# Performance work log

Measured on AMD Instinct MI355X. Metric: run time of the kernel, lower is better.

The kernel has to match this reference:

```python
import jax, jax.numpy as jnp
import numpy as np

# module constants (from init_kwargs)
OUT_W = 22
OUT_H = 48
IN_H = 64
IN_W = 44
DT_OFF = 0.5
DX_OFF = 0.5
DY_OFF = 0.5
SIGMA_OFF = 1.0
DELTA_T_OFF = 1.0
DELTA_OFF = 1.0
EPS = 1e-8
ATT_H = int(round(OUT_W / IN_W * IN_H))  # 32

N, C, T, H, W = 16, 64, 30, 64, 44


def setup_inputs() -> dict:
    key = jax.random.key(0)
    ks = jax.random.split(key, 8)
    inp = {"x": jax.random.normal(ks[0], (N, C, T, H, W), dtype=jnp.float32)}
    names = ["dt", "dx", "dy", "log_sigma2", "log_delta_t", "log_delta", "log_gamma"]
    for i, nm in enumerate(names):
        inp[nm] = jax.random.normal(ks[i + 1], (N, 1), dtype=jnp.float32)
    return inp


def _filterbank(mu, grid_len, sigma2):
    # mu: [N, out_len]; sigma2: [N,1,1] -> F: [N, out_len, grid_len], row-normalized
    g = jnp.arange(grid_len, dtype=jnp.float32)  # [grid_len]
    F = jnp.exp(-((g[None, None, :] - mu[:, :, None]) ** 2) / (2.0 * sigma2))
    return F / jnp.maximum(F.sum(axis=2, keepdims=True), EPS)


def reference(x, dt, dx, dy, log_sigma2, log_delta_t, log_delta, log_gamma):
    n, c, t, h, w = x.shape
    anchor_t, anchor_x, anchor_y = t * DT_OFF, w * DX_OFF, h * DY_OFF

    dt_ = jnp.tanh(dt) * t / 2.0 + anchor_t          # [N,1]
    dx_ = jnp.tanh(dx) * IN_W / 2.0 + anchor_x
    dy_ = jnp.tanh(dy) * IN_H / 2.0 + anchor_y
    sigma2 = (jnp.exp(log_sigma2) * SIGMA_OFF).reshape(-1, 1, 1)
    delta_t = jnp.exp(log_delta_t) * DELTA_T_OFF
    delta = jnp.exp(log_delta) * DELTA_OFF
    gamma = jax.nn.sigmoid(log_gamma)

    gt = jnp.arange(t, dtype=jnp.float32)[None, :]
    gx = jnp.arange(OUT_W, dtype=jnp.float32)[None, :]
    gy = jnp.arange(ATT_H, dtype=jnp.float32)[None, :]
    mu_t = dt_ + (gt - t / 2.0) * delta_t            # [N,T]
    mu_x = dx_ + (gx - OUT_W / 2.0) * delta          # [N,out_w]
    mu_y = dy_ + (gy - ATT_H / 2.0) * delta          # [N,att_h]

    Ft = _filterbank(mu_t, t, sigma2)                # [N,T,T]
    Fx = _filterbank(mu_x, w, sigma2)                # [N,out_w,W]
    Fy = _filterbank(mu_y, h, sigma2)                # [N,att_h,H]

    # glimpse = Ft @ (Fy @ x @ Fx^T) over appropriate axes
    g = jnp.einsum('ncthw,naw->nctha', x, Fx)        # [N,C,T,H,out_w]
    g = jnp.einsum('nctha,nbh->nctba', g, Fy)        # [N,C,T,att_h,out_w]
    g = jnp.einsum('nctba,nst->ncsba', g, Ft)        # [N,C,T,att_h,out_w]

    out = g * gamma.reshape(-1, 1, 1, 1, 1)
    pad_t = (OUT_H - ATT_H) // 2
    pad_b = OUT_H - pad_t - ATT_H
    out = jnp.pad(out, ((0, 0), (0, 0), (0, 0), (pad_t, pad_b), (0, 0)))
    return out
```

## Files before the change

### kernel.cpp

```cpp
#include <hip/hip_runtime.h>
#include <hip/hip_fp16.h>

#define XN 16
#define XC 64
#define XT 30
#define XH 64
#define XW 44
#define OUTW 22
#define ATTH 32
#define OUTH 48
#define SLICE (XH*XW)
#define OSLICE (OUTH*OUTW)

#define WS_FX 0
#define WS_FY (3*64*4)
#define WS_FT (WS_FY + 4*64*4)
#define WS_N  (WS_FT + 2*64*4)

typedef _Float16 f16;
typedef f16 f16x8 __attribute__((ext_vector_type(8)));
typedef float f32x16 __attribute__((ext_vector_type(16)));
typedef float f32x4 __attribute__((ext_vector_type(4)));

__device__ __forceinline__ unsigned int PK(float a, float b) {
    return __builtin_bit_cast(unsigned int, __builtin_amdgcn_cvt_pkrtz(a, b));
}
__device__ __forceinline__ f32x16 MF(uint4 a, uint4 b, f32x16 c) {
    return __builtin_amdgcn_mfma_f32_32x32x16_f16(
        __builtin_bit_cast(f16x8, a), __builtin_bit_cast(f16x8, b), c, 0, 0, 0);
}
__device__ __forceinline__ f32x16 ZF() {
    f32x16 z;
    #pragma unroll
    for (int i = 0; i < 16; ++i) z[i] = 0.f;
    return z;
}

__global__ void prep_kernel(const float* __restrict__ dtp, const float* __restrict__ dxp,
                            const float* __restrict__ dyp, const float* __restrict__ ls2,
                            const float* __restrict__ ldt, const float* __restrict__ ldp,
                            unsigned int* __restrict__ ws)
{
    __shared__ float fx[22][44];
    __shared__ float fy[32][64];
    __shared__ float ft[30][32];
    const int n = blockIdx.x;
    const int r = threadIdx.x;
    const float dt_ = tanhf(dtp[n]) * 15.f + 15.f;
    const float dx_ = tanhf(dxp[n]) * 22.f + 22.f;
    const float dy_ = tanhf(dyp[n]) * 32.f + 32.f;
    const float inv2s = 1.f / (2.f * expf(ls2[n]));
    const float delta_t = expf(ldt[n]);
    const float delta = expf(ldp[n]);

    if (r < 30) {
        float mu = dt_ + (float)(r - 15) * delta_t;
        float e[30]; float sum = 0.f;
        for (int t = 0; t < 30; ++t) { float d = (float)t - mu; float v = expf(-d*d*inv2s); e[t] = v; sum += v; }
        float inv = 1.f / fmaxf(sum, 1e-8f);
        for (int t = 0; t < 30; ++t) ft[r][t] = e[t] * inv;
        ft[r][30] = 0.f; ft[r][31] = 0.f;
    } else if (r < 52) {
        int a = r - 30;
        float mu = dx_ + (float)(a - 11) * delta;
        float e[44]; float sum = 0.f;
        for (int w = 0; w < 44; ++w) { float d = (float)w - mu; float v = expf(-d*d*inv2s); e[w] = v; sum += v; }
        float inv = 1.f / fmaxf(sum, 1e-8f);
        for (int w = 0; w < 44; ++w) fx[a][w] = e[w] * inv;
    } else if (r < 84) {
        int b = r - 52;
        float mu = dy_ + (float)(b - 16) * delta;
        float e[64]; float sum = 0.f;
        for (int h = 0; h < 64; ++h) { float d = (float)h - mu; float v = expf(-d*d*inv2s); e[h] = v; sum += v; }
        float inv = 1.f / fmaxf(sum, 1e-8f);
        for (int h = 0; h < 64; ++h) fy[b][h] = e[h] * inv;
    }
    __syncthreads();

    if (r < 64) {
        const int al = r & 31, hf = r >> 5;
        unsigned int* wn = ws + n * WS_N;
        #pragma unroll
        for (int kt = 0; kt < 3; ++kt) {
            int w0 = kt*16 + 8*hf;
            float v[8];
            #pragma unroll
            for (int i = 0; i < 8; ++i) { int w = w0 + i; v[i] = (al < 22 && w < 44) ? fx[al][w] : 0.f; }
            #pragma unroll
            for (int j = 0; j < 4; ++j) {
                unsigned int lo = __half_as_ushort(__float2half_rn(v[2*j]));
                unsigned int hi = __half_as_ushort(__float2half_rn(v[2*j+1]));
                wn[WS_FX + (kt*64 + r)*4 + j] = lo | (hi << 16);
            }
        }
        #pragma unroll
        for (int kt = 0; kt < 4; ++kt) {
            int h0 = kt*16 + 8*hf;
            float v[8];
            #pragma unroll
            for (int i = 0; i < 8; ++i) v[i] = fy[al][h0 + i];
            #pragma unroll
            for (int j = 0; j < 4; ++j) {
                unsigned int lo = __half_as_ushort(__float2half_rn(v[2*j]));
                unsigned int hi = __half_as_ushort(__float2half_rn(v[2*j+1]));
                wn[WS_FY + (kt*64 + r)*4 + j] = lo | (hi << 16);
            }
        }
        #pragma unroll
        for (int kt = 0; kt < 2; ++kt) {
            int t0 = kt*16 + 8*hf;
            float v[8];
            #pragma unroll
            for (int i = 0; i < 8; ++i) v[i] = (al < 30) ? ft[al][t0 + i] : 0.f;
            #pragma unroll
            for (int j = 0; j < 4; ++j) {
                unsigned int lo = __half_as_ushort(__float2half_rn(v[2*j]));
                unsigned int hi = __half_as_ushort(__float2half_rn(v[2*j+1]));
                wn[WS_FT + (kt*64 + r)*4 + j] = lo | (hi << 16);
            }
        }
    }
}

__global__ __launch_bounds__(256, 3) void glimpse_kernel(
    const float* __restrict__ x, const unsigned int* __restrict__ ws,
    const float* __restrict__ p_lg, float* __restrict__ out)
{
    const int tid = threadIdx.x;
    const int n = blockIdx.x >> 6, c = blockIdx.x & 63;
    const int wv = tid >> 6, l = tid & 63;
    const int al = l & 31, hf = l >> 5;

    __shared__ unsigned int a2t[704*17];

    for (int r = tid; r < 704; r += 256) { a2t[r*17 + 15] = 0u; a2t[r*17 + 16] = 0u; }

    const size_t obase = (size_t)(n*XC + c) * (XT*OSLICE);
    {
        f32x4 z4 = {0.f, 0.f, 0.f, 0.f};
        f32x4* out4 = (f32x4*)(out + obase);
        #pragma unroll
        for (int k2 = 0; k2 < 11; ++k2) {
            int idx = tid + k2*256;
            if (idx < 2640) {
                int s = idx / 88;
                int rr = idx - s*88;
                int j = (rr < 44) ? rr : (rr + 176);
                __builtin_nontemporal_store(z4, out4 + s*264 + j);
            }
        }
    }

    const unsigned int* wn = ws + n * WS_N;
    uint4 fxf[3], fyf[4], ftf[2];
    #pragma unroll
    for (int kt = 0; kt < 3; ++kt) fxf[kt] = *(const uint4*)(wn + WS_FX + (kt*64 + l)*4);
    #pragma unroll
    for (int kt = 0; kt < 4; ++kt) fyf[kt] = *(const uint4*)(wn + WS_FY + (kt*64 + l)*4);
    #pragma unroll
    for (int kt = 0; kt < 2; ++kt) ftf[kt] = *(const uint4*)(wn + WS_FT + (kt*64 + l)*4);

    const float gamma = 1.f / (1.f + expf(-p_lg[n]));

    unsigned short* a2t16 = (unsigned short*)a2t;
    const float* xc = x + (size_t)(n*XC + c) * (XT*SLICE);

    #pragma unroll 1
    for (int t = wv; t < XT; t += 4) {
        const float* xs = xc + (size_t)t * SLICE;
        const float* rb0 = xs + al*44;
        const float* rb1 = xs + (32 + al)*44;
        float4 A0a = *(const float4*)(rb0 + 8*hf);
        float4 A1a = *(const float4*)(rb0 + 8*hf + 4);
        float4 B0a = *(const float4*)(rb0 + 16 + 8*hf);
        float4 B1a = *(const float4*)(rb0 + 16 + 8*hf + 4);
        float4 C0a = *(const float4*)(rb0 + 32 + 8*hf);
        float4 C1a = (hf == 0) ? *(const float4*)(rb0 + 36) : make_float4(0.f,0.f,0.f,0.f);
        float4 A0b = *(const float4*)(rb1 + 8*hf);
        float4 A1b = *(const float4*)(rb1 + 8*hf + 4);
        float4 B0b = *(const float4*)(rb1 + 16 + 8*hf);
        float4 B1b = *(const float4*)(rb1 + 16 + 8*hf + 4);
        float4 C0b = *(const float4*)(rb1 + 32 + 8*hf);
        float4 C1b = (hf == 0) ? *(const float4*)(rb1 + 36) : make_float4(0.f,0.f,0.f,0.f);

        f32x16 D0 = ZF(), D1m = ZF(), D2 = ZF();
        {
            uint4 u0 = make_uint4(PK(A0a.x,A0a.y), PK(A0a.z,A0a.w), PK(A1a.x,A1a.y), PK(A1a.z,A1a.w));
            uint4 u1 = make_uint4(PK(B0a.x,B0a.y), PK(B0a.z,B0a.w), PK(B1a.x,B1a.y), PK(B1a.z,B1a.w));
            uint4 u2 = make_uint4(PK(C0a.x,C0a.y), PK(C0a.z,C0a.w), PK(C1a.x,C1a.y), PK(C1a.z,C1a.w));
            D0 = MF(u0, fxf[0], D0); D0 = MF(u1, fxf[1], D0); D0 = MF(u2, fxf[2], D0);
        }
        {
            uint4 u0 = make_uint4(PK(A0b.x,A0b.y), PK(A0b.z,A0b.w), PK(A1b.x,A1b.y), PK(A1b.z,A1b.w));
            uint4 u1 = make_uint4(PK(B0b.x,B0b.y), PK(B0b.z,B0b.w), PK(B1b.x,B1b.y), PK(B1b.z,B1b.w));
            uint4 u2 = make_uint4(PK(C0b.x,C0b.y), PK(C0b.z,C0b.w), PK(C1b.x,C1b.y), PK(C1b.z,C1b.w));
            D1m = MF(u0, fxf[0], D1m); D1m = MF(u1, fxf[1], D1m); D1m = MF(u2, fxf[2], D1m);
        }

        #pragma unroll
        for (int half = 0; half < 2; ++half) {
            const f32x16& D = half ? D1m : D0;
            unsigned int w0g[4], w1g[4];
            #pragma unroll
            for (int g = 0; g < 4; ++g) {
                w0g[g] = PK(D[4*g],   D[4*g+1]);
                w1g[g] = PK(D[4*g+2], D[4*g+3]);
            }
            #pragma unroll
            for (int ktl = 0; ktl < 2; ++ktl) {
                const int gA = 2*ktl, gB = 2*ktl + 1;
                unsigned int own0 = hf ? w0g[gB] : w0g[gA];
                unsigned int own1 = hf ? w1g[gB] : w1g[gA];
                unsigned int snd0 = hf ? w0g[gA] : w0g[gB];
                unsigned int snd1 = hf ? w1g[gA] : w1g[gB];
                unsigned int rcv0 = (unsigned int)__shfl_xor((int)snd0, 32, 64);
                unsigned int rcv1 = (unsigned int)__shfl_xor((int)snd1, 32, 64);
                uint4 frag;
                frag.x = hf ? rcv0 : own0;
                frag.y = hf ? rcv1 : own1;
                frag.z = hf ? own0 : rcv0;
                frag.w = hf ? own1 : rcv1;
                D2 = MF(fyf[half*2 + ktl], frag, D2);
            }
        }

        if (al < 22) {
            #pragma unroll
            for (int q = 0; q < 16; ++q) {
                int b = (q & 3) + 8*(q >> 2) + 4*hf;
                unsigned short hv = __builtin_bit_cast(unsigned short, (_Float16)D2[q]);
                a2t16[(b*22 + al)*34 + t] = hv;
            }
        }
    }
    __syncthreads();

    #pragma unroll 2
    for (int nt = wv; nt < 22; nt += 4) {
        int ba = nt*32 + al;
        f32x16 D3 = ZF();
        #pragma unroll
        for (int kt = 0; kt < 2; ++kt) {
            int base = ba*17 + kt*8 + 4*hf;
            uint4 bw;
            bw.x = a2t[base]; bw.y = a2t[base+1]; bw.z = a2t[base+2]; bw.w = a2t[base+3];
            D3 = MF(ftf[kt], bw, D3);
        }
        float* ob = out + obase + 176 + ba;
        #pragma unroll
        for (int q = 0; q < 16; ++q) {
            int s = (q & 3) + 8*(q >> 2) + 4*hf;
            if (s < XT) __builtin_nontemporal_store(gamma * D3[q], ob + s*OSLICE);
        }
    }
}

extern "C" void kernel_launch(void* const* d_in, const int* in_sizes, int n_in,
                              void* d_out, int out_size, void* d_ws, size_t ws_size,
                              hipStream_t stream) {
    const float* x   = (const float*)d_in[0];
    const float* dt  = (const float*)d_in[1];
    const float* dx  = (const float*)d_in[2];
    const float* dy  = (const float*)d_in[3];
    const float* ls2 = (const float*)d_in[4];
    const float* ldt = (const float*)d_in[5];
    const float* ld  = (const float*)d_in[6];
    const float* lg  = (const float*)d_in[7];
    float* out = (float*)d_out;
    unsigned int* ws = (unsigned int*)d_ws;

    prep_kernel<<<dim3(XN), dim3(96), 0, stream>>>(dt, dx, dy, ls2, ldt, ld, ws);
    glimpse_kernel<<<dim3(XN * XC), dim3(256), 0, stream>>>(x, ws, lg, out);
}
```

Baseline: 116.5 us.

## Coalesce x loads, prefetch next slice, stage through swizzled per-wave LDS

Each wave now loads its T-slice of x as fully coalesced float4 chunks (11 per lane), packs them to fp16 and writes them into a per-wave swizzled LDS tile. The MFMA A-operands are then read back from LDS instead of coming from strided row-wise global loads. The next slice's loads are issued before the current slice is processed, as a register double-buffer. This is meant to remove uncoalesced global access and hide load latency, at the cost of extra LDS traffic and more registers, which is why the occupancy hint drops from 3 to 2 blocks.

```diff
diff --git a/kernel.cpp b/kernel.cpp
--- a/kernel.cpp
+++ b/kernel.cpp
@@ -122,7 +122,7 @@
     }
 }
 
-__global__ __launch_bounds__(256, 3) void glimpse_kernel(
+__global__ __launch_bounds__(256, 2) void glimpse_kernel(
     const float* __restrict__ x, const unsigned int* __restrict__ ws,
     const float* __restrict__ p_lg, float* __restrict__ out)
 {
@@ -131,9 +131,15 @@
     const int wv = tid >> 6, l = tid & 63;
     const int al = l & 31, hf = l >> 5;
 
-    __shared__ unsigned int a2t[704*17];
+    __shared__ unsigned int lds_all[4*1024 + 704*17];
+    unsigned int* xst = lds_all + wv * 1024;
+    unsigned int* a2t = lds_all + 4096;
 
     for (int r = tid; r < 704; r += 256) { a2t[r*17 + 15] = 0u; a2t[r*17 + 16] = 0u; }
+    if (l < 32) {
+        int ph = l*32 + ((5 ^ (l & 7)) << 2) + 2;
+        xst[ph] = 0u; xst[ph + 1] = 0u;
+    }
 
     const size_t obase = (size_t)(n*XC + c) * (XT*OSLICE);
     {
@@ -165,35 +171,60 @@
     unsigned short* a2t16 = (unsigned short*)a2t;
     const float* xc = x + (size_t)(n*XC + c) * (XT*SLICE);
 
+    float4 v[11];
+    {
+        const float4* src = (const float4*)(xc + (size_t)wv * SLICE);
+        #pragma unroll
+        for (int k = 0; k < 11; ++k) v[k] = src[k*64 + l];
+    }
+
     #pragma unroll 1
     for (int t = wv; t < XT; t += 4) {
-        const float* xs = xc + (size_t)t * SLICE;
-        const float* rb0 = xs + al*44;
-        const float* rb1 = xs + (32 + al)*44;
-        float4 A0a = *(const float4*)(rb0 + 8*hf);
-        float4 A1a = *(const float4*)(rb0 + 8*hf + 4);
-        float4 B0a = *(const float4*)(rb0 + 16 + 8*hf);
-        float4 B1a = *(const float4*)(rb0 + 16 + 8*hf + 4);
-        float4 C0a = *(const float4*)(rb0 + 32 + 8*hf);
-        float4 C1a = (hf == 0) ? *(const float4*)(rb0 + 36) : make_float4(0.f,0.f,0.f,0.f);
-        float4 A0b = *(const float4*)(rb1 + 8*hf);
-        float4 A1b = *(const float4*)(rb1 + 8*hf + 4);
-        float4 B0b = *(const float4*)(rb1 + 16 + 8*hf);
-        float4 B1b = *(const float4*)(rb1 + 16 + 8*hf + 4);
-        float4 C0b = *(const float4*)(rb1 + 32 + 8*hf);
-        float4 C1b = (hf == 0) ? *(const float4*)(rb1 + 36) : make_float4(0.f,0.f,0.f,0.f);
+        unsigned int pk[22];
+        #pragma unroll
+        for (int k = 0; k < 11; ++k) {
+            pk[2*k]   = PK(v[k].x, v[k].y);
+            pk[2*k+1] = PK(v[k].z, v[k].w);
+        }
+        if (t + 4 < XT) {
+            const float4* src = (const float4*)(xc + (size_t)(t+4) * SLICE);
+            #pragma unroll
+            for (int k = 0; k < 11; ++k) v[k] = src[k*64 + l];
+        }
 
         f32x16 D0 = ZF(), D1m = ZF(), D2 = ZF();
+        #pragma unroll
+        for (int k = 0; k < 6; ++k) {
+            int flat = k*64 + l;
+            if (k < 5 || l < 32) {
+                int r = flat / 11;
+                int m = flat - r*11;
+                int ph = (r & 31)*32 + (((m >> 1) ^ (r & 7)) << 2) + ((m & 1) << 1);
+                uint2 pr; pr.x = pk[2*k]; pr.y = pk[2*k+1];
+                *(uint2*)(xst + ph) = pr;
+            }
+        }
         {
-            uint4 u0 = make_uint4(PK(A0a.x,A0a.y), PK(A0a.z,A0a.w), PK(A1a.x,A1a.y), PK(A1a.z,A1a.w));
-            uint4 u1 = make_uint4(PK(B0a.x,B0a.y), PK(B0a.z,B0a.w), PK(B1a.x,B1a.y), PK(B1a.z,B1a.w));
-            uint4 u2 = make_uint4(PK(C0a.x,C0a.y), PK(C0a.z,C0a.w), PK(C1a.x,C1a.y), PK(C1a.z,C1a.w));
+            uint4 u0 = *(const uint4*)(xst + al*32 + (((0 + hf) ^ (al & 7)) << 2));
+            uint4 u1 = *(const uint4*)(xst + al*32 + (((2 + hf) ^ (al & 7)) << 2));
+            uint4 u2 = *(const uint4*)(xst + al*32 + (((4 + hf) ^ (al & 7)) << 2));
             D0 = MF(u0, fxf[0], D0); D0 = MF(u1, fxf[1], D0); D0 = MF(u2, fxf[2], D0);
         }
+        #pragma unroll
+        for (int k = 5; k < 11; ++k) {
+            int flat = k*64 + l;
+            if (k > 5 || l >= 32) {
+                int r = flat / 11;
+                int m = flat - r*11;
+                int ph = (r & 31)*32 + (((m >> 1) ^ (r & 7)) << 2) + ((m & 1) << 1);
+                uint2 pr; pr.x = pk[2*k]; pr.y = pk[2*k+1];
+                *(uint2*)(xst + ph) = pr;
+            }
+        }
         {
-            uint4 u0 = make_uint4(PK(A0b.x,A0b.y), PK(A0b.z,A0b.w), PK(A1b.x,A1b.y), PK(A1b.z,A1b.w));
-            uint4 u1 = make_uint4(PK(B0b.x,B0b.y), PK(B0b.z,B0b.w), PK(B1b.x,B1b.y), PK(B1b.z,B1b.w));
-            uint4 u2 = make_uint4(PK(C0b.x,C0b.y), PK(C0b.z,C0b.w), PK(C1b.x,C1b.y), PK(C1b.z,C1b.w));
+            uint4 u0 = *(const uint4*)(xst + al*32 + (((0 + hf) ^ (al & 7)) << 2));
+            uint4 u1 = *(const uint4*)(xst + al*32 + (((2 + hf) ^ (al & 7)) << 2));
+            uint4 u2 = *(const uint4*)(xst + al*32 + (((4 + hf) ^ (al & 7)) << 2));
             D1m = MF(u0, fxf[0], D1m); D1m = MF(u1, fxf[1], D1m); D1m = MF(u2, fxf[2], D1m);
         }
 
```

New measurement: 113.1 us. -2.9%, faster.

## Use 512-thread blocks and batch two time-slice loads per wave

Applied to the files above, without the earlier changes.

Doubles the block to 8 waves, so each (n,c) block spreads its 30 time slices over more waves. Each wave now issues the global loads for two time slices (t and t+8) up front before running the MFMA chain on either, which adds memory-level parallelism and hides load latency. The cost is higher register pressure from holding 24 float4s per thread, plus a launch-bounds change to 2 blocks of 512 threads that may limit occupancy or cause spills.

```diff
diff --git a/kernel.cpp b/kernel.cpp
--- a/kernel.cpp
+++ b/kernel.cpp
@@ -122,7 +122,7 @@
     }
 }
 
-__global__ __launch_bounds__(256, 3) void glimpse_kernel(
+__global__ __launch_bounds__(512, 2) void glimpse_kernel(
     const float* __restrict__ x, const unsigned int* __restrict__ ws,
     const float* __restrict__ p_lg, float* __restrict__ out)
 {
@@ -133,15 +133,15 @@
 
     __shared__ unsigned int a2t[704*17];
 
-    for (int r = tid; r < 704; r += 256) { a2t[r*17 + 15] = 0u; a2t[r*17 + 16] = 0u; }
+    for (int r = tid; r < 704; r += 512) { a2t[r*17 + 15] = 0u; a2t[r*17 + 16] = 0u; }
 
     const size_t obase = (size_t)(n*XC + c) * (XT*OSLICE);
     {
         f32x4 z4 = {0.f, 0.f, 0.f, 0.f};
         f32x4* out4 = (f32x4*)(out + obase);
         #pragma unroll
-        for (int k2 = 0; k2 < 11; ++k2) {
-            int idx = tid + k2*256;
+        for (int k2 = 0; k2 < 6; ++k2) {
+            int idx = tid + k2*512;
             if (idx < 2640) {
                 int s = idx / 88;
                 int rr = idx - s*88;
@@ -166,77 +166,111 @@
     const float* xc = x + (size_t)(n*XC + c) * (XT*SLICE);
 
     #pragma unroll 1
-    for (int t = wv; t < XT; t += 4) {
-        const float* xs = xc + (size_t)t * SLICE;
-        const float* rb0 = xs + al*44;
-        const float* rb1 = xs + (32 + al)*44;
-        float4 A0a = *(const float4*)(rb0 + 8*hf);
-        float4 A1a = *(const float4*)(rb0 + 8*hf + 4);
-        float4 B0a = *(const float4*)(rb0 + 16 + 8*hf);
-        float4 B1a = *(const float4*)(rb0 + 16 + 8*hf + 4);
-        float4 C0a = *(const float4*)(rb0 + 32 + 8*hf);
-        float4 C1a = (hf == 0) ? *(const float4*)(rb0 + 36) : make_float4(0.f,0.f,0.f,0.f);
-        float4 A0b = *(const float4*)(rb1 + 8*hf);
-        float4 A1b = *(const float4*)(rb1 + 8*hf + 4);
-        float4 B0b = *(const float4*)(rb1 + 16 + 8*hf);
-        float4 B1b = *(const float4*)(rb1 + 16 + 8*hf + 4);
-        float4 C0b = *(const float4*)(rb1 + 32 + 8*hf);
-        float4 C1b = (hf == 0) ? *(const float4*)(rb1 + 36) : make_float4(0.f,0.f,0.f,0.f);
-
-        f32x16 D0 = ZF(), D1m = ZF(), D2 = ZF();
+    for (int si = 0; si < 2; ++si) {
+        const int tA = wv + si*16;
+        const int tB = tA + 8;
+        const bool doB = (tB < XT);
+
+        float4 LA0, LA1, LA2, LA3, LA4, LA5, LA6, LA7, LA8, LA9, LA10, LA11;
+        float4 LB0, LB1, LB2, LB3, LB4, LB5, LB6, LB7, LB8, LB9, LB10, LB11;
         {
-            uint4 u0 = make_uint4(PK(A0a.x,A0a.y), PK(A0a.z,A0a.w), PK(A1a.x,A1a.y), PK(A1a.z,A1a.w));
-            uint4 u1 = make_uint4(PK(B0a.x,B0a.y), PK(B0a.z,B0a.w), PK(B1a.x,B1a.y), PK(B1a.z,B1a.w));
-            uint4 u2 = make_uint4(PK(C0a.x,C0a.y), PK(C0a.z,C0a.w), PK(C1a.x,C1a.y), PK(C1a.z,C1a.w));
-            D0 = MF(u0, fxf[0], D0); D0 = MF(u1, fxf[1], D0); D0 = MF(u2, fxf[2], D0);
-        }
-        {
-            uint4 u0 = make_uint4(PK(A0b.x,A0b.y), PK(A0b.z,A0b.w), PK(A1b.x,A1b.y), PK(A1b.z,A1b.w));
-            uint4 u1 = make_uint4(PK(B0b.x,B0b.y), PK(B0b.z,B0b.w), PK(B1b.x,B1b.y), PK(B1b.z,B1b.w));
-            uint4 u2 = make_uint4(PK(C0b.x,C0b.y), PK(C0b.z,C0b.w), PK(C1b.x,C1b.y), PK(C1b.z,C1b.w));
-            D1m = MF(u0, fxf[0], D1m); D1m = MF(u1, fxf[1], D1m); D1m = MF(u2, fxf[2], D1m);
-        }
-
-        #pragma unroll
-        for (int half = 0; half < 2; ++half) {
-            const f32x16& D = half ? D1m : D0;
-            unsigned int w0g[4], w1g[4];
-            #pragma unroll
-            for (int g = 0; g < 4; ++g) {
-                w0g[g] = PK(D[4*g],   D[4*g+1]);
-                w1g[g] = PK(D[4*g+2], D[4*g+3]);
-            }
-            #pragma unroll
-            for (int ktl = 0; ktl < 2; ++ktl) {
-                const int gA = 2*ktl, gB = 2*ktl + 1;
-                unsigned int own0 = hf ? w0g[gB] : w0g[gA];
-                unsigned int own1 = hf ? w1g[gB] : w1g[gA];
-                unsigned int snd0 = hf ? w0g[gA] : w0g[gB];
-                unsigned int snd1 = hf ? w1g[gA] : w1g[gB];
-                unsigned int rcv0 = (unsigned int)__shfl_xor((int)snd0, 32, 64);
-                unsigned int rcv1 = (unsigned int)__shfl_xor((int)snd1, 32, 64);
-                uint4 frag;
-                frag.x = hf ? rcv0 : own0;
-                frag.y = hf ? rcv1 : own1;
-                frag.z = hf ? own0 : rcv0;
-                frag.w = hf ? own1 : rcv1;
-                D2 = MF(fyf[half*2 + ktl], frag, D2);
-            }
-        }
-
-        if (al < 22) {
-            #pragma unroll
-            for (int q = 0; q < 16; ++q) {
-                int b = (q & 3) + 8*(q >> 2) + 4*hf;
-                unsigned short hv = __builtin_bit_cast(unsigned short, (_Float16)D2[q]);
-                a2t16[(b*22 + al)*34 + t] = hv;
+            const float* rb0 = xc + (size_t)tA * SLICE + al*44;
+            const float* rb1 = rb0 + 32*44;
+            LA0 = *(const float4*)(rb0 + 8*hf);
+            LA1 = *(const float4*)(rb0 + 8*hf + 4);
+            LA2 = *(const float4*)(rb0 + 16 + 8*hf);
+            LA3 = *(const float4*)(rb0 + 16 + 8*hf + 4);
+            LA4 = *(const float4*)(rb0 + 32 + 8*hf);
+            LA5 = (hf == 0) ? *(const float4*)(rb0 + 36) : make_float4(0.f,0.f,0.f,0.f);
+            LA6 = *(const float4*)(rb1 + 8*hf);
+            LA7 = *(const float4*)(rb1 + 8*hf + 4);
+            LA8 = *(const float4*)(rb1 + 16 + 8*hf);
+            LA9 = *(const float4*)(rb1 + 16 + 8*hf + 4);
+            LA10 = *(const float4*)(rb1 + 32 + 8*hf);
+            LA11 = (hf == 0) ? *(const float4*)(rb1 + 36) : make_float4(0.f,0.f,0.f,0.f);
+        }
+        if (doB) {
+            const float* rb0 = xc + (size_t)tB * SLICE + al*44;
+            const float* rb1 = rb0 + 32*44;
+            LB0 = *(const float4*)(rb0 + 8*hf);
+            LB1 = *(const float4*)(rb0 + 8*hf + 4);
+            LB2 = *(const float4*)(rb0 + 16 + 8*hf);
+            LB3 = *(const float4*)(rb0 + 16 + 8*hf + 4);
+            LB4 = *(const float4*)(rb0 + 32 + 8*hf);
+            LB5 = (hf == 0) ? *(const float4*)(rb0 + 36) : make_float4(0.f,0.f,0.f,0.f);
+            LB6 = *(const float4*)(rb1 + 8*hf);
+            LB7 = *(const float4*)(rb1 + 8*hf + 4);
+            LB8 = *(const float4*)(rb1 + 16 + 8*hf);
+            LB9 = *(const float4*)(rb1 + 16 + 8*hf + 4);
+            LB10 = *(const float4*)(rb1 + 32 + 8*hf);
+            LB11 = (hf == 0) ? *(const float4*)(rb1 + 36) : make_float4(0.f,0.f,0.f,0.f);
+        }
+
+        #pragma unroll
+        for (int sl = 0; sl < 2; ++sl) {
+            if (sl == 1 && !doB) break;
+            const int t = sl ? tB : tA;
+            f32x16 D0 = ZF(), D1m = ZF(), D2 = ZF();
+            {
+                float4 a0 = sl ? LB0 : LA0,  a1 = sl ? LB1 : LA1;
+                float4 a2 = sl ? LB2 : LA2,  a3 = sl ? LB3 : LA3;
+                float4 a4 = sl ? LB4 : LA4,  a5 = sl ? LB5 : LA5;
+                uint4 u0 = make_uint4(PK(a0.x,a0.y), PK(a0.z,a0.w), PK(a1.x,a1.y), PK(a1.z,a1.w));
+                uint4 u1 = make_uint4(PK(a2.x,a2.y), PK(a2.z,a2.w), PK(a3.x,a3.y), PK(a3.z,a3.w));
+                uint4 u2 = make_uint4(PK(a4.x,a4.y), PK(a4.z,a4.w), PK(a5.x,a5.y), PK(a5.z,a5.w));
+                D0 = MF(u0, fxf[0], D0); D0 = MF(u1, fxf[1], D0); D0 = MF(u2, fxf[2], D0);
+            }
+            {
+                float4 a0 = sl ? LB6 : LA6,  a1 = sl ? LB7 : LA7;
+                float4 a2 = sl ? LB8 : LA8,  a3 = sl ? LB9 : LA9;
+                float4 a4 = sl ? LB10 : LA10, a5 = sl ? LB11 : LA11;
+                uint4 u0 = make_uint4(PK(a0.x,a0.y), PK(a0.z,a0.w), PK(a1.x,a1.y), PK(a1.z,a1.w));
+                uint4 u1 = make_uint4(PK(a2.x,a2.y), PK(a2.z,a2.w), PK(a3.x,a3.y), PK(a3.z,a3.w));
+                uint4 u2 = make_uint4(PK(a4.x,a4.y), PK(a4.z,a4.w), PK(a5.x,a5.y), PK(a5.z,a5.w));
+                D1m = MF(u0, fxf[0], D1m); D1m = MF(u1, fxf[1], D1m); D1m = MF(u2, fxf[2], D1m);
+            }
+
+            #pragma unroll
+            for (int half = 0; half < 2; ++half) {
+                const f32x16& D = half ? D1m : D0;
+                unsigned int w0g[4], w1g[4];
+                #pragma unroll
+                for (int g = 0; g < 4; ++g) {
+                    w0g[g] = PK(D[4*g],   D[4*g+1]);
+                    w1g[g] = PK(D[4*g+2], D[4*g+3]);
+                }
+                #pragma unroll
+                for (int ktl = 0; ktl < 2; ++ktl) {
+                    const int gA = 2*ktl, gB = 2*ktl + 1;
+                    unsigned int own0 = hf ? w0g[gB] : w0g[gA];
+                    unsigned int own1 = hf ? w1g[gB] : w1g[gA];
+                    unsigned int snd0 = hf ? w0g[gA] : w0g[gB];
+                    unsigned int snd1 = hf ? w1g[gA] : w1g[gB];
+                    unsigned int rcv0 = (unsigned int)__shfl_xor((int)snd0, 32, 64);
+                    unsigned int rcv1 = (unsigned int)__shfl_xor((int)snd1, 32, 64);
+                    uint4 frag;
+                    frag.x = hf ? rcv0 : own0;
+                    frag.y = hf ? rcv1 : own1;
+                    frag.z = hf ? own0 : rcv0;
+                    frag.w = hf ? own1 : rcv1;
+                    D2 = MF(fyf[half*2 + ktl], frag, D2);
+                }
+            }
+
+            if (al < 22) {
+                #pragma unroll
+                for (int q = 0; q < 16; ++q) {
+                    int b = (q & 3) + 8*(q >> 2) + 4*hf;
+                    unsigned short hv = __builtin_bit_cast(unsigned short, (_Float16)D2[q]);
+                    a2t16[(b*22 + al)*34 + t] = hv;
+                }
             }
         }
     }
     __syncthreads();
 
-    #pragma unroll 2
-    for (int nt = wv; nt < 22; nt += 4) {
+    #pragma unroll 1
+    for (int nt = wv; nt < 22; nt += 8) {
         int ba = nt*32 + al;
         f32x16 D3 = ZF();
         #pragma unroll
@@ -270,5 +304,5 @@
     unsigned int* ws = (unsigned int*)d_ws;
 
     prep_kernel<<<dim3(XN), dim3(96), 0, stream>>>(dt, dx, dy, ls2, ldt, ld, ws);
-    glimpse_kernel<<<dim3(XN * XC), dim3(256), 0, stream>>>(x, ws, lg, out);
-}
+    glimpse_kernel<<<dim3(XN * XC), dim3(512), 0, stream>>>(x, ws, lg, out);
+}
```

New measurement: 110.2 us. 5.4% less time.
